# Kernel tuning notes

Hardware: AMD Instinct MI355X
Metric: run time of the kernel (lower is better)

## Reference

```python
import jax, jax.numpy as jnp
import numpy as np
import math

B, L, DIM, DEPTH, HEADS, DH, T, BUCKETS, MAXDIST = 256, 77, 768, 12, 12, 64, 1000, 32, 128
INNER = HEADS * DH            # 768
FF_IN = 4 * DIM               # 3072 (SwiGLU inner)
EPS = 1e-5


def rmsnorm(x, gamma):
    inv = jax.lax.rsqrt(jnp.sum(x * x, axis=-1, keepdims=True) + EPS)
    return x * inv * gamma * (DIM ** 0.5)


def rel_pos_bias(i, j, table):
    # table: [BUCKETS, HEADS] -> bias [HEADS, i, j]
    q_pos = jnp.arange(i)
    k_pos = jnp.arange(j)
    rel = k_pos[None, :] - q_pos[:, None]
    n = jnp.maximum(-rel, 0)
    max_exact = BUCKETS // 2
    is_small = n < max_exact
    nf = jnp.maximum(n, 1).astype(jnp.float32)
    val_large = max_exact + (jnp.log(nf / max_exact) / math.log(MAXDIST / max_exact) * (BUCKETS - max_exact)).astype(jnp.int32)
    val_large = jnp.minimum(val_large, BUCKETS - 1)
    bucket = jnp.where(is_small, n, val_large)
    return jnp.transpose(table[bucket], (2, 0, 1))  # h i j


def attention(x, mask, bias, gamma, Wq, Wkv, Wout, null_kv):
    b, n, _ = x.shape
    xn = rmsnorm(x, gamma)
    q = (xn @ Wq).reshape(b, n, HEADS, DH).transpose(0, 2, 1, 3)     # b h n d
    kv = xn @ Wkv                                                     # b n 2d (single head)
    k, v = kv[..., :DH], kv[..., DH:]
    nk = jnp.broadcast_to(null_kv[0], (b, 1, DH))
    nv = jnp.broadcast_to(null_kv[1], (b, 1, DH))
    k = jnp.concatenate([nk, k], axis=1)                              # b (n+1) d
    v = jnp.concatenate([nv, v], axis=1)
    sim = jnp.einsum('bhid,bjd->bhij', q * (DH ** -0.5), k) + bias[None]
    neg = -jnp.finfo(sim.dtype).max
    m = jnp.pad(mask, ((0, 0), (1, 0)), constant_values=True)         # null kv always visible
    sim = jnp.where(m[:, None, None, :], sim, neg)
    i, j = n, n + 1
    causal = jnp.arange(j)[None, :] > (jnp.arange(i)[:, None] + (j - i))
    sim = jnp.where(causal[None, None], neg, sim)
    attn = jax.nn.softmax(sim - jax.lax.stop_gradient(sim.max(axis=-1, keepdims=True)), axis=-1)
    out = jnp.einsum('bhij,bjd->bhid', attn, v)
    out = out.transpose(0, 2, 1, 3).reshape(b, n, INNER)
    return out @ Wout


def feedforward(x, gamma, W1, W2):
    h = rmsnorm(x, gamma) @ W1                                        # b n 2*FF_IN
    a, gate = h[..., :FF_IN], h[..., FF_IN:]
    return (a * jax.nn.silu(gate)) @ W2


def setup_inputs() -> dict:
    key = jax.random.key(0)
    ks = jax.random.split(key, 16)
    s = 0.02
    return {
        'image_embed': jax.random.normal(ks[0], (B, DIM), jnp.float32),
        'text_encodings': jax.random.normal(ks[1], (B, L, DIM), jnp.float32),
        'text_embed': jax.random.normal(ks[2], (B, DIM), jnp.float32),
        'time_emb_table': jax.random.normal(ks[3], (T, DIM), jnp.float32) * s,
        'learned_query': jax.random.normal(ks[4], (DIM,), jnp.float32),
        'rel_bias_table': jax.random.normal(ks[5], (BUCKETS, HEADS), jnp.float32) * s,
        'attn_gamma': jnp.ones((DEPTH, DIM), jnp.float32),
        'Wq': jax.random.normal(ks[6], (DEPTH, DIM, INNER), jnp.float32) * s,
        'Wkv': jax.random.normal(ks[7], (DEPTH, DIM, 2 * DH), jnp.float32) * s,
        'Wout': jax.random.normal(ks[8], (DEPTH, INNER, DIM), jnp.float32) * s,
        'null_kv': jax.random.normal(ks[9], (DEPTH, 2, DH), jnp.float32),
        'ff_gamma': jnp.ones((DEPTH, DIM), jnp.float32),
        'Wff1': jax.random.normal(ks[10], (DEPTH, DIM, 2 * FF_IN), jnp.float32) * s,
        'Wff2': jax.random.normal(ks[11], (DEPTH, FF_IN, DIM), jnp.float32) * s,
        'diffusion_timesteps': jax.random.randint(ks[12], (B,), 0, T),
        'mask': jnp.ones((B, L), dtype=bool),
    }


def reference(image_embed, text_encodings, text_embed, time_emb_table, learned_query,
              rel_bias_table, attn_gamma, Wq, Wkv, Wout, null_kv, ff_gamma, Wff1, Wff2,
              diffusion_timesteps, mask):
    b = image_embed.shape[0]
    # mask bookkeeping (matches torch forward); cond_drop_prob fixed at 1.0 -> keep all
    not_all = jnp.any(mask, axis=-1)
    m = jnp.concatenate([mask, not_all[:, None]], axis=1)
    m = jnp.pad(m, ((0, 0), (0, 2)), constant_values=True)            # [b, L+3]
    time_embed = time_emb_table[diffusion_timesteps][:, None, :]
    queries = jnp.broadcast_to(learned_query, (b, 1, DIM))
    tokens = jnp.concatenate([text_encodings, text_embed[:, None, :], time_embed, queries], axis=1)
    n = tokens.shape[1]
    bias = rel_pos_bias(n, n + 1, rel_bias_table)
    x = tokens
    for l in range(DEPTH):
        x = attention(x, m, bias, attn_gamma[l], Wq[l], Wkv[l], Wout[l], null_kv[l]) + x
        x = feedforward(x, ff_gamma[l], Wff1[l], Wff2[l]) + x
    return x[:, -1, :]
```

## Files before the change

### kernel.cpp

```cpp
#include <hip/hip_runtime.h>
#include <hip/hip_bf16.h>
#include <float.h>
#include <math.h>

#define NB 256
#define LTXT 77
#define DIM 768
#define DEPTH 12
#define HEADS 12
#define DH 64
#define NTOK 80
#define NKEY 81
#define NROWS (NB*NTOK)
#define FFH 3072
#define FF2C 6144
#define INNER 768
#define SROW 100

typedef __hip_bfloat16 bf16;
typedef __attribute__((ext_vector_type(8))) short short8;
typedef __attribute__((ext_vector_type(4))) float f32x4;

__device__ __forceinline__ unsigned short f2bf(float f) {
    __hip_bfloat16 h = __float2bfloat16(f);
    return __builtin_bit_cast(unsigned short, h);
}

__global__ void build_tokens(const float* __restrict__ text_enc,
                             const float* __restrict__ text_emb,
                             const float* __restrict__ time_tab,
                             const float* __restrict__ lquery,
                             const int* __restrict__ tsteps,
                             float* __restrict__ x) {
    int idx = blockIdx.x * 256 + threadIdx.x;
    if (idx >= NROWS * DIM) return;
    int d = idx % DIM;
    int row = idx / DIM;
    int b = row / NTOK, p = row % NTOK;
    float v;
    if (p < LTXT)            v = text_enc[((size_t)b * LTXT + p) * DIM + d];
    else if (p == LTXT)      v = text_emb[(size_t)b * DIM + d];
    else if (p == LTXT + 1)  v = time_tab[(size_t)tsteps[b] * DIM + d];
    else                     v = lquery[d];
    x[idx] = v;
}

__global__ void build_biasR(const float* __restrict__ table, float* __restrict__ biasR) {
    int idx = blockIdx.x * 256 + threadIdx.x;
    if (idx >= HEADS * NTOK * 96) return;
    int kap = idx % 96;
    int i = (idx / 96) % NTOK;
    int h = idx / (96 * NTOK);
    float v;
    if ((kap < 80 && kap > i) || kap > 80) {
        v = -1e30f;
    } else {
        int j = (kap < 80) ? kap + 1 : 0;
        int rel = j - i;
        int n = rel < 0 ? -rel : 0;
        int bucket;
        if (n < 16) {
            bucket = n;
        } else {
            float val = logf((float)n / 16.0f) / logf(8.0f) * 16.0f;
            int vl = 16 + (int)val;
            bucket = vl < 31 ? vl : 31;
        }
        v = table[bucket * HEADS + h];
    }
    biasR[idx] = v;
}

__global__ __launch_bounds__(256) void convT(const float* __restrict__ W,
                                             bf16* __restrict__ WT,
                                             int K, int N) {
    __shared__ float t[32][33];
    int n0 = blockIdx.x * 32, k0 = blockIdx.y * 32;
    int tx = threadIdx.x & 31, ty = threadIdx.x >> 5;
    #pragma unroll
    for (int i = 0; i < 4; i++)
        t[ty + 8 * i][tx] = W[(size_t)(k0 + ty + 8 * i) * N + n0 + tx];
    __syncthreads();
    #pragma unroll
    for (int i = 0; i < 4; i++)
        WT[(size_t)(n0 + ty + 8 * i) * K + k0 + tx] = __float2bfloat16(t[tx][ty + 8 * i]);
}

__global__ __launch_bounds__(256) void rmsnorm_w(const float* __restrict__ x,
                                                 const float* __restrict__ gamma,
                                                 bf16* __restrict__ out) {
    int wave = blockIdx.x * 4 + (threadIdx.x >> 6);
    int lane = threadIdx.x & 63;
    float4 g0 = *(const float4*)&gamma[lane * 4];
    float4 g1 = *(const float4*)&gamma[lane * 4 + 256];
    float4 g2 = *(const float4*)&gamma[lane * 4 + 512];
    #pragma unroll 2
    for (int rr = 0; rr < 8; ++rr) {
        int row = wave * 8 + rr;
        const float* xr = x + (size_t)row * DIM + lane * 4;
        float4 v0 = *(const float4*)xr;
        float4 v1 = *(const float4*)(xr + 256);
        float4 v2 = *(const float4*)(xr + 512);
        float ss = v0.x*v0.x + v0.y*v0.y + v0.z*v0.z + v0.w*v0.w
                 + v1.x*v1.x + v1.y*v1.y + v1.z*v1.z + v1.w*v1.w
                 + v2.x*v2.x + v2.y*v2.y + v2.z*v2.z + v2.w*v2.w;
        #pragma unroll
        for (int o = 32; o > 0; o >>= 1) ss += __shfl_xor(ss, o);
        float inv = 27.712812921102035f / sqrtf(ss + 1e-5f);
        bf16* orow = out + (size_t)row * DIM + lane * 4;
        ushort4 w0 = { f2bf(v0.x*inv*g0.x), f2bf(v0.y*inv*g0.y), f2bf(v0.z*inv*g0.z), f2bf(v0.w*inv*g0.w) };
        ushort4 w1 = { f2bf(v1.x*inv*g1.x), f2bf(v1.y*inv*g1.y), f2bf(v1.z*inv*g1.z), f2bf(v1.w*inv*g1.w) };
        ushort4 w2 = { f2bf(v2.x*inv*g2.x), f2bf(v2.y*inv*g2.y), f2bf(v2.z*inv*g2.z), f2bf(v2.w*inv*g2.w) };
        *(ushort4*)(orow)       = w0;
        *(ushort4*)(orow + 256) = w1;
        *(ushort4*)(orow + 512) = w2;
    }
}


#define STAGE_LOAD(dst, base, b0, ld)                                          \
    _Pragma("unroll")                                                          \
    for (int r_ = 0; r_ < 4; ++r_) {                                           \
        int idx_ = r_ * 256 + t;                                               \
        int row_ = idx_ >> 3, c_ = idx_ & 7;                                   \
        dst[r_] = *(const short8*)&base[(size_t)(b0 + row_) * ld + k0 + c_ * 8];\
    }

#define STAGE_WRITE(lds, src)                                                  \
    _Pragma("unroll")                                                          \
    for (int r_ = 0; r_ < 4; ++r_) {                                           \
        int idx_ = r_ * 256 + t;                                               \
        int row_ = idx_ >> 3, c_ = idx_ & 7;                                   \
        *(short8*)((char*)lds + row_ * 128 + ((c_ ^ (row_ & 7)) << 4)) = src[r_];\
    }

#define FRAG_READ(dst, lds, base_row, kk)                                      \
    _Pragma("unroll")                                                          \
    for (int q_ = 0; q_ < 4; ++q_) {                                           \
        int row_ = (base_row) + q_ * 16 + fr;                                  \
        dst[q_] = *(const short8*)((const char*)lds + row_ * 128 +             \
                     ((((kk << 2) + kb) ^ (row_ & 7)) << 4));                  \
    }

template<int EPI>
__global__ __launch_bounds__(256) void gemm_bt(const bf16* __restrict__ A,
                                               const bf16* __restrict__ BT,
                                               float* __restrict__ C,
                                               int N, int K) {
    __shared__ __align__(16) short As[128 * 64];
    __shared__ __align__(16) short Bs[128 * 64];
    const int t = threadIdx.x;
    const int lane = t & 63;
    const int wid = t >> 6;
    const int wr = wid >> 1, wc = wid & 1;
    const int fr = lane & 15;
    const int kb = lane >> 4;
    const int row0 = blockIdx.y * 128, col0 = blockIdx.x * 128;

    f32x4 acc[4][4] = {};
    short8 ra[4], rb[4];
    const int NKT = K >> 6;

    int k0 = 0;
    STAGE_LOAD(ra, A, row0, K)
    STAGE_LOAD(rb, BT, col0, K)
    STAGE_WRITE(As, ra)
    STAGE_WRITE(Bs, rb)
    __syncthreads();

    for (int kt = 1; kt < NKT; ++kt) {
        k0 = kt << 6;
        STAGE_LOAD(ra, A, row0, K)
        STAGE_LOAD(rb, BT, col0, K)
        #pragma unroll
        for (int kk = 0; kk < 2; ++kk) {
            short8 af[4], bv[4];
            FRAG_READ(af, As, wr * 64, kk)
            FRAG_READ(bv, Bs, wc * 64, kk)
            #pragma unroll
            for (int i = 0; i < 4; ++i)
                #pragma unroll
                for (int j = 0; j < 4; ++j)
                    acc[i][j] = __builtin_amdgcn_mfma_f32_16x16x32_bf16(af[i], bv[j], acc[i][j], 0, 0, 0);
        }
        __syncthreads();
        STAGE_WRITE(As, ra)
        STAGE_WRITE(Bs, rb)
        __syncthreads();
    }
    #pragma unroll
    for (int kk = 0; kk < 2; ++kk) {
        short8 af[4], bv[4];
        FRAG_READ(af, As, wr * 64, kk)
        FRAG_READ(bv, Bs, wc * 64, kk)
        #pragma unroll
        for (int i = 0; i < 4; ++i)
            #pragma unroll
            for (int j = 0; j < 4; ++j)
                acc[i][j] = __builtin_amdgcn_mfma_f32_16x16x32_bf16(af[i], bv[j], acc[i][j], 0, 0, 0);
    }

    #pragma unroll
    for (int i = 0; i < 4; ++i) {
        #pragma unroll
        for (int j = 0; j < 4; ++j) {
            int row = row0 + wr * 64 + i * 16 + kb * 4;
            int col = col0 + wc * 64 + j * 16 + fr;
            #pragma unroll
            for (int r = 0; r < 4; ++r) {
                size_t o = (size_t)(row + r) * N + col;
                if (EPI == 1)      C[o] += acc[i][j][r];
                else               ((bf16*)C)[o] = __float2bfloat16(acc[i][j][r]);
            }
        }
    }
}

__global__ __launch_bounds__(256) void gemm_kv(const bf16* __restrict__ A,
                                               const bf16* __restrict__ BT,
                                               bf16* __restrict__ kb,
                                               bf16* __restrict__ vT) {
    __shared__ __align__(16) short As[128 * 64];
    __shared__ __align__(16) short Bs[128 * 64];
    const int t = threadIdx.x;
    const int lane = t & 63;
    const int wid = t >> 6;
    const int wr = wid >> 1, wc = wid & 1;
    const int fr = lane & 15;
    const int kb_ = lane >> 4;
    const int row0 = blockIdx.y * 128, col0 = 0;
    const int K = DIM, N = 128;
    #define kb_frag kb_

    f32x4 acc[4][4] = {};
    short8 ra[4], rb[4];

    int k0 = 0;
    STAGE_LOAD(ra, A, row0, K)
    STAGE_LOAD(rb, BT, col0, K)
    STAGE_WRITE(As, ra)
    STAGE_WRITE(Bs, rb)
    __syncthreads();

    for (int kt = 1; kt < (DIM >> 6); ++kt) {
        k0 = kt << 6;
        STAGE_LOAD(ra, A, row0, K)
        STAGE_LOAD(rb, BT, col0, K)
        #pragma unroll
        for (int kk = 0; kk < 2; ++kk) {
            short8 af[4], bv[4];
            {
                _Pragma("unroll")
                for (int q_ = 0; q_ < 4; ++q_) {
                    int row_ = wr * 64 + q_ * 16 + fr;
                    af[q_] = *(const short8*)((const char*)As + row_ * 128 + ((((kk << 2) + kb_) ^ (row_ & 7)) << 4));
                }
                _Pragma("unroll")
                for (int q_ = 0; q_ < 4; ++q_) {
                    int row_ = wc * 64 + q_ * 16 + fr;
                    bv[q_] = *(const short8*)((const char*)Bs + row_ * 128 + ((((kk << 2) + kb_) ^ (row_ & 7)) << 4));
                }
            }
            #pragma unroll
            for (int i = 0; i < 4; ++i)
                #pragma unroll
                for (int j = 0; j < 4; ++j)
                    acc[i][j] = __builtin_amdgcn_mfma_f32_16x16x32_bf16(af[i], bv[j], acc[i][j], 0, 0, 0);
        }
        __syncthreads();
        STAGE_WRITE(As, ra)
        STAGE_WRITE(Bs, rb)
        __syncthreads();
    }
    #pragma unroll
    for (int kk = 0; kk < 2; ++kk) {
        short8 af[4], bv[4];
        _Pragma("unroll")
        for (int q_ = 0; q_ < 4; ++q_) {
            int row_ = wr * 64 + q_ * 16 + fr;
            af[q_] = *(const short8*)((const char*)As + row_ * 128 + ((((kk << 2) + kb_) ^ (row_ & 7)) << 4));
        }
        _Pragma("unroll")
        for (int q_ = 0; q_ < 4; ++q_) {
            int row_ = wc * 64 + q_ * 16 + fr;
            bv[q_] = *(const short8*)((const char*)Bs + row_ * 128 + ((((kk << 2) + kb_) ^ (row_ & 7)) << 4));
        }
        #pragma unroll
        for (int i = 0; i < 4; ++i)
            #pragma unroll
            for (int j = 0; j < 4; ++j)
                acc[i][j] = __builtin_amdgcn_mfma_f32_16x16x32_bf16(af[i], bv[j], acc[i][j], 0, 0, 0);
    }

    #pragma unroll
    for (int i = 0; i < 4; ++i) {
        #pragma unroll
        for (int j = 0; j < 4; ++j) {
            int row = row0 + wr * 64 + i * 16 + kb_ * 4;
            int col = wc * 64 + j * 16 + fr;
            #pragma unroll
            for (int r = 0; r < 4; ++r) {
                int rg = row + r;
                float v = acc[i][j][r];
                if (wc == 0) {
                    kb[(size_t)rg * 64 + col] = __float2bfloat16(v);
                } else {
                    int bb = rg / NTOK, ii = rg - bb * NTOK;
                    vT[((size_t)bb * 64 + (col - 64)) * NTOK + ii] = __float2bfloat16(v);
                }
            }
        }
    }
    #undef kb_frag
}

__global__ __launch_bounds__(256) void attn_mfma(const bf16* __restrict__ qb,
                                                 const bf16* __restrict__ kbuf,
                                                 const bf16* __restrict__ vT,
                                                 const float* __restrict__ nullkv,
                                                 const float* __restrict__ biasR,
                                                 bf16* __restrict__ attnb) {
    const int b = blockIdx.x / HEADS;
    const int h = blockIdx.x % HEADS;
    __shared__ __align__(16) short Ks[96 * 64];
    __shared__ __align__(16) short Vt[64 * 128];
    __shared__ __align__(16) float Sls[80 * SROW];
    char* Sb = (char*)Sls;
    const int t = threadIdx.x;
    const int lane = t & 63;
    const int wid = t >> 6;
    const int g = lane >> 4;
    const int fr = lane & 15;

    for (int c = t; c < 768; c += 256) {
        int row = c >> 3, ch = c & 7;
        short8 v;
        if (row < NTOK) {
            v = *(const short8*)&kbuf[((size_t)(b * NTOK + row)) * 64 + ch * 8];
        } else if (row == NTOK) {
            #pragma unroll
            for (int e = 0; e < 8; ++e) v[e] = (short)f2bf(nullkv[ch * 8 + e]);
        } else {
            v = short8{0,0,0,0,0,0,0,0};
        }
        *(short8*)((char*)Ks + row * 128 + ((ch ^ (row & 7)) << 4)) = v;
    }
    for (int c = t; c < 1024; c += 256) {
        int d = c >> 4, ch = c & 15;
        if (ch >= 12) continue;
        short8 v;
        if (ch < 10) {
            v = *(const short8*)&vT[((size_t)b * 64 + d) * NTOK + ch * 8];
        } else if (ch == 10) {
            v = short8{0,0,0,0,0,0,0,0};
            v[0] = (short)f2bf(nullkv[64 + d]);
        } else {
            v = short8{0,0,0,0,0,0,0,0};
        }
        *(short8*)((char*)Vt + d * 256 + ((ch ^ (d & 7)) << 4)) = v;
    }
    __syncthreads();

    const bf16* qbase = qb + ((size_t)(b * NTOK)) * INNER + h * DH;
    for (int s = 0; s < 8; ++s) {
        int tt = wid + 4 * s;
        if (tt >= 30) break;
        int m = tt / 6, n = tt - 6 * m;
        f32x4 acc = {};
        #pragma unroll
        for (int kk = 0; kk < 2; ++kk) {
            short8 a = *(const short8*)&qbase[(size_t)(m * 16 + fr) * INNER + kk * 32 + g * 8];
            int krow = n * 16 + fr;
            short8 kf = *(const short8*)((const char*)Ks + krow * 128 + ((((kk << 2) + g) ^ (krow & 7)) << 4));
            acc = __builtin_amdgcn_mfma_f32_16x16x32_bf16(a, kf, acc, 0, 0, 0);
        }
        int i0 = m * 16 + g * 4;
        int kap = n * 16 + fr;
        const float* bR = biasR + ((size_t)h * NTOK + i0) * 96 + kap;
        #pragma unroll
        for (int r = 0; r < 4; ++r)
            Sls[(i0 + r) * SROW + kap] = acc[r] * 0.125f + bR[r * 96];
    }
    __syncthreads();

    for (int rr = 0; rr < 20; ++rr) {
        int row = wid + 4 * rr;
        const float* Srow = Sls + row * SROW;
        float s0 = Srow[lane];
        float s1v = Srow[64 + (lane & 31)];
        float mx = fmaxf(s0, s1v);
        #pragma unroll
        for (int o = 32; o > 0; o >>= 1) mx = fmaxf(mx, __shfl_xor(mx, o));
        float e0 = __expf(s0 - mx);
        float e1 = (lane < 32) ? __expf(s1v - mx) : 0.0f;
        float sum = e0 + e1;
        #pragma unroll
        for (int o = 32; o > 0; o >>= 1) sum += __shfl_xor(sum, o);
        float inv = 1.0f / sum;
        *(unsigned short*)(Sb + row * (SROW * 4) + lane * 2) = f2bf(e0 * inv);
        if (lane < 32)
            *(unsigned short*)(Sb + row * (SROW * 4) + 128 + lane * 2) = f2bf(e1 * inv);
    }
    __syncthreads();

    for (int s = 0; s < 5; ++s) {
        int tt = wid + 4 * s;
        int m = tt >> 2, n = tt & 3;
        f32x4 acc = {};
        #pragma unroll
        for (int kc = 0; kc < 3; ++kc) {
            short8 p = *(const short8*)(Sb + (m * 16 + fr) * (SROW * 4) + kc * 64 + g * 16);
            int drow = n * 16 + fr;
            short8 vv = *(const short8*)((const char*)Vt + drow * 256 + ((((kc << 2) + g) ^ (drow & 7)) << 4));
            acc = __builtin_amdgcn_mfma_f32_16x16x32_bf16(p, vv, acc, 0, 0, 0);
        }
        int i0 = m * 16 + g * 4;
        int d = n * 16 + fr;
        #pragma unroll
        for (int r = 0; r < 4; ++r)
            attnb[((size_t)(b * NTOK) + i0 + r) * INNER + h * DH + d] = __float2bfloat16(acc[r]);
    }
}

__global__ __launch_bounds__(256) void gemm_ff1(const bf16* __restrict__ A,
                                                const bf16* __restrict__ W1T,
                                                bf16* __restrict__ act) {
    __shared__ __align__(16) short As[128 * 64];
    __shared__ __align__(16) short Bs1[128 * 64];
    __shared__ __align__(16) short Bs2[128 * 64];
    const int t = threadIdx.x;
    const int lane = t & 63;
    const int wid = t >> 6;
    const int wr = wid >> 1, wc = wid & 1;
    const int fr = lane & 15;
    const int kb = lane >> 4;
    const int row0 = blockIdx.y * 128, col0 = blockIdx.x * 128;
    const int K = DIM;
    const bf16* B1 = W1T;
    const bf16* B2 = W1T + (size_t)FFH * DIM;

    f32x4 acc1[4][4] = {}, acc2[4][4] = {};
    short8 ra[4], rb1[4], rb2[4];

    int k0 = 0;
    STAGE_LOAD(ra, A, row0, K)
    STAGE_LOAD(rb1, B1, col0, K)
    STAGE_LOAD(rb2, B2, col0, K)
    STAGE_WRITE(As, ra)
    STAGE_WRITE(Bs1, rb1)
    STAGE_WRITE(Bs2, rb2)
    __syncthreads();

    for (int kt = 1; kt < (DIM >> 6); ++kt) {
        k0 = kt << 6;
        STAGE_LOAD(ra, A, row0, K)
        STAGE_LOAD(rb1, B1, col0, K)
        STAGE_LOAD(rb2, B2, col0, K)
        #pragma unroll
        for (int kk = 0; kk < 2; ++kk) {
            short8 af[4], b1v[4], b2v[4];
            FRAG_READ(af, As, wr * 64, kk)
            FRAG_READ(b1v, Bs1, wc * 64, kk)
            FRAG_READ(b2v, Bs2, wc * 64, kk)
            #pragma unroll
            for (int i = 0; i < 4; ++i)
                #pragma unroll
                for (int j = 0; j < 4; ++j) {
                    acc1[i][j] = __builtin_amdgcn_mfma_f32_16x16x32_bf16(af[i], b1v[j], acc1[i][j], 0, 0, 0);
                    acc2[i][j] = __builtin_amdgcn_mfma_f32_16x16x32_bf16(af[i], b2v[j], acc2[i][j], 0, 0, 0);
                }
        }
        __syncthreads();
        STAGE_WRITE(As, ra)
        STAGE_WRITE(Bs1, rb1)
        STAGE_WRITE(Bs2, rb2)
        __syncthreads();
    }
    #pragma unroll
    for (int kk = 0; kk < 2; ++kk) {
        short8 af[4], b1v[4], b2v[4];
        FRAG_READ(af, As, wr * 64, kk)
        FRAG_READ(b1v, Bs1, wc * 64, kk)
        FRAG_READ(b2v, Bs2, wc * 64, kk)
        #pragma unroll
        for (int i = 0; i < 4; ++i)
            #pragma unroll
            for (int j = 0; j < 4; ++j) {
                acc1[i][j] = __builtin_amdgcn_mfma_f32_16x16x32_bf16(af[i], b1v[j], acc1[i][j], 0, 0, 0);
                acc2[i][j] = __builtin_amdgcn_mfma_f32_16x16x32_bf16(af[i], b2v[j], acc2[i][j], 0, 0, 0);
            }
    }

    #pragma unroll
    for (int i = 0; i < 4; ++i) {
        #pragma unroll
        for (int j = 0; j < 4; ++j) {
            int row = row0 + wr * 64 + i * 16 + kb * 4;
            int col = col0 + wc * 64 + j * 16 + fr;
            #pragma unroll
            for (int r = 0; r < 4; ++r) {
                float a = acc1[i][j][r];
                float gt = acc2[i][j][r];
                float s = a * gt / (1.0f + __expf(-gt));
                act[(size_t)(row + r) * FFH + col] = __float2bfloat16(s);
            }
        }
    }
}

__global__ void extract(const float* __restrict__ x, float* __restrict__ out) {
    int idx = blockIdx.x * 256 + threadIdx.x;
    if (idx >= NB * DIM) return;
    int b = idx / DIM, d = idx % DIM;
    out[idx] = x[((size_t)(b * NTOK + NTOK - 1)) * DIM + d];
}

extern "C" void kernel_launch(void* const* d_in, const int* in_sizes, int n_in,
                              void* d_out, int out_size, void* d_ws, size_t ws_size,
                              hipStream_t stream) {
    (void)in_sizes; (void)n_in; (void)out_size; (void)ws_size;
    const float* text_enc = (const float*)d_in[1];
    const float* text_emb = (const float*)d_in[2];
    const float* time_tab = (const float*)d_in[3];
    const float* lquery   = (const float*)d_in[4];
    const float* rel_tab  = (const float*)d_in[5];
    const float* attn_g   = (const float*)d_in[6];
    const float* Wq       = (const float*)d_in[7];
    const float* Wkv      = (const float*)d_in[8];
    const float* Wout     = (const float*)d_in[9];
    const float* null_kv  = (const float*)d_in[10];
    const float* ff_g     = (const float*)d_in[11];
    const float* Wff1     = (const float*)d_in[12];
    const float* Wff2     = (const float*)d_in[13];
    const int*   tsteps   = (const int*)d_in[14];

    char* ws = (char*)d_ws;
    float* x     = (float*)(ws);
    bf16*  xn    = (bf16*)(ws + 62914560);
    bf16*  attnb = xn;
    char*  U     = ws + 94371840;
    bf16*  qb    = (bf16*)U;
    bf16*  kbuf  = (bf16*)(U + 31457280);
    bf16*  vT    = (bf16*)(U + 34078720);
    bf16*  act   = (bf16*)U;
    float* biasR = (float*)(ws + 220200960);
    bf16*  WqT   = (bf16*)(ws + 220569600);
    bf16*  WkvT  = (bf16*)(ws + 221749248);
    bf16*  WoutT = (bf16*)(ws + 221945856);
    bf16*  Wff1T = (bf16*)(ws + 223125504);
    bf16*  Wff2T = (bf16*)(ws + 232562688);

    build_tokens<<<(NROWS * DIM + 255) / 256, 256, 0, stream>>>(text_enc, text_emb, time_tab, lquery, tsteps, x);
    build_biasR<<<(HEADS * NTOK * 96 + 255) / 256, 256, 0, stream>>>(rel_tab, biasR);

    for (int l = 0; l < DEPTH; l++) {
        convT<<<dim3(INNER / 32, DIM / 32), 256, 0, stream>>>(Wq   + (size_t)l * DIM * INNER,  WqT,   DIM,   INNER);
        convT<<<dim3((2 * DH) / 32, DIM / 32), 256, 0, stream>>>(Wkv + (size_t)l * DIM * 2 * DH, WkvT, DIM, 2 * DH);
        convT<<<dim3(DIM / 32, INNER / 32), 256, 0, stream>>>(Wout + (size_t)l * INNER * DIM,  WoutT, INNER, DIM);
        convT<<<dim3(FF2C / 32, DIM / 32), 256, 0, stream>>>(Wff1 + (size_t)l * DIM * FF2C,    Wff1T, DIM,   FF2C);
        convT<<<dim3(DIM / 32, FFH / 32), 256, 0, stream>>>(Wff2  + (size_t)l * FFH * DIM,     Wff2T, FFH,   DIM);

        rmsnorm_w<<<NROWS / (8 * 4), 256, 0, stream>>>(x, attn_g + (size_t)l * DIM, xn);
        gemm_bt<2><<<dim3(INNER / 128, NROWS / 128), 256, 0, stream>>>(xn, WqT, (float*)qb, INNER, DIM);
        gemm_kv<<<dim3(1, NROWS / 128), 256, 0, stream>>>(xn, WkvT, kbuf, vT);
        attn_mfma<<<NB * HEADS, 256, 0, stream>>>(qb, kbuf, vT, null_kv + (size_t)l * 2 * DH, biasR, attnb);
        gemm_bt<1><<<dim3(DIM / 128, NROWS / 128), 256, 0, stream>>>(attnb, WoutT, x, DIM, INNER);

        rmsnorm_w<<<NROWS / (8 * 4), 256, 0, stream>>>(x, ff_g + (size_t)l * DIM, xn);
        gemm_ff1<<<dim3(FFH / 128, NROWS / 128), 256, 0, stream>>>(xn, Wff1T, act);
        gemm_bt<1><<<dim3(DIM / 128, NROWS / 128), 256, 0, stream>>>(act, Wff2T, x, DIM, FFH);
    }

    extract<<<(NB * DIM + 255) / 256, 256, 0, stream>>>(x, (float*)d_out);
}
```

Baseline: 9.137 ms.

## Load GEMM tiles directly into LDS with global_load_lds, dropping register prefetch

```diff
diff --git a/kernel.cpp b/kernel.cpp
--- a/kernel.cpp
+++ b/kernel.cpp
@@ -118,28 +118,25 @@
 }
 
 
-#define STAGE_LOAD(dst, base, b0, ld)                                          \
+#define GSTAGE(lds, base, b0, ld)                                              \
     _Pragma("unroll")                                                          \
     for (int r_ = 0; r_ < 4; ++r_) {                                           \
         int idx_ = r_ * 256 + t;                                               \
         int row_ = idx_ >> 3, c_ = idx_ & 7;                                   \
-        dst[r_] = *(const short8*)&base[(size_t)(b0 + row_) * ld + k0 + c_ * 8];\
-    }
-
-#define STAGE_WRITE(lds, src)                                                  \
-    _Pragma("unroll")                                                          \
-    for (int r_ = 0; r_ < 4; ++r_) {                                           \
-        int idx_ = r_ * 256 + t;                                               \
-        int row_ = idx_ >> 3, c_ = idx_ & 7;                                   \
-        *(short8*)((char*)lds + row_ * 128 + ((c_ ^ (row_ & 7)) << 4)) = src[r_];\
+        int cs_ = c_ ^ (row_ & 7);                                             \
+        __builtin_amdgcn_global_load_lds(                                      \
+            (const __attribute__((address_space(1))) unsigned int*)            \
+                &base[(size_t)(b0 + row_) * ld + k0 + cs_ * 8],                \
+            (__attribute__((address_space(3))) unsigned int*)&lds[idx_ * 8],   \
+            16, 0, 0);                                                         \
     }
 
 #define FRAG_READ(dst, lds, base_row, kk)                                      \
     _Pragma("unroll")                                                          \
     for (int q_ = 0; q_ < 4; ++q_) {                                           \
         int row_ = (base_row) + q_ * 16 + fr;                                  \
-        dst[q_] = *(const short8*)((const char*)lds + row_ * 128 +             \
-                     ((((kk << 2) + kb) ^ (row_ & 7)) << 4));                  \
+        int ch_ = ((((kk) << 2) + kb) ^ (row_ & 7));                           \
+        dst[q_] = *(const short8*)&lds[row_ * 64 + ch_ * 8];                   \
     }
 
 template<int EPI>
@@ -158,20 +155,13 @@
     const int row0 = blockIdx.y * 128, col0 = blockIdx.x * 128;
 
     f32x4 acc[4][4] = {};
-    short8 ra[4], rb[4];
     const int NKT = K >> 6;
 
-    int k0 = 0;
-    STAGE_LOAD(ra, A, row0, K)
-    STAGE_LOAD(rb, BT, col0, K)
-    STAGE_WRITE(As, ra)
-    STAGE_WRITE(Bs, rb)
-    __syncthreads();
-
-    for (int kt = 1; kt < NKT; ++kt) {
-        k0 = kt << 6;
-        STAGE_LOAD(ra, A, row0, K)
-        STAGE_LOAD(rb, BT, col0, K)
+    for (int kt = 0; kt < NKT; ++kt) {
+        int k0 = kt << 6;
+        GSTAGE(As, A, row0, K)
+        GSTAGE(Bs, BT, col0, K)
+        __syncthreads();
         #pragma unroll
         for (int kk = 0; kk < 2; ++kk) {
             short8 af[4], bv[4];
@@ -184,20 +174,6 @@
                     acc[i][j] = __builtin_amdgcn_mfma_f32_16x16x32_bf16(af[i], bv[j], acc[i][j], 0, 0, 0);
         }
         __syncthreads();
-        STAGE_WRITE(As, ra)
-        STAGE_WRITE(Bs, rb)
-        __syncthreads();
-    }
-    #pragma unroll
-    for (int kk = 0; kk < 2; ++kk) {
-        short8 af[4], bv[4];
-        FRAG_READ(af, As, wr * 64, kk)
-        FRAG_READ(bv, Bs, wc * 64, kk)
-        #pragma unroll
-        for (int i = 0; i < 4; ++i)
-            #pragma unroll
-            for (int j = 0; j < 4; ++j)
-                acc[i][j] = __builtin_amdgcn_mfma_f32_16x16x32_bf16(af[i], bv[j], acc[i][j], 0, 0, 0);
     }
 
     #pragma unroll
@@ -218,7 +194,7 @@
 
 __global__ __launch_bounds__(256) void gemm_kv(const bf16* __restrict__ A,
                                                const bf16* __restrict__ BT,
-                                               bf16* __restrict__ kb,
+                                               bf16* __restrict__ kout,
                                                bf16* __restrict__ vT) {
     __shared__ __align__(16) short As[128 * 64];
     __shared__ __align__(16) short Bs[128 * 64];
@@ -227,40 +203,22 @@
     const int wid = t >> 6;
     const int wr = wid >> 1, wc = wid & 1;
     const int fr = lane & 15;
-    const int kb_ = lane >> 4;
-    const int row0 = blockIdx.y * 128, col0 = 0;
-    const int K = DIM, N = 128;
-    #define kb_frag kb_
+    const int kb = lane >> 4;
+    const int row0 = blockIdx.y * 128;
+    const int K = DIM;
 
     f32x4 acc[4][4] = {};
-    short8 ra[4], rb[4];
-
-    int k0 = 0;
-    STAGE_LOAD(ra, A, row0, K)
-    STAGE_LOAD(rb, BT, col0, K)
-    STAGE_WRITE(As, ra)
-    STAGE_WRITE(Bs, rb)
-    __syncthreads();
-
-    for (int kt = 1; kt < (DIM >> 6); ++kt) {
-        k0 = kt << 6;
-        STAGE_LOAD(ra, A, row0, K)
-        STAGE_LOAD(rb, BT, col0, K)
+
+    for (int kt = 0; kt < (DIM >> 6); ++kt) {
+        int k0 = kt << 6;
+        GSTAGE(As, A, row0, K)
+        GSTAGE(Bs, BT, 0, K)
+        __syncthreads();
         #pragma unroll
         for (int kk = 0; kk < 2; ++kk) {
             short8 af[4], bv[4];
-            {
-                _Pragma("unroll")
-                for (int q_ = 0; q_ < 4; ++q_) {
-                    int row_ = wr * 64 + q_ * 16 + fr;
-                    af[q_] = *(const short8*)((const char*)As + row_ * 128 + ((((kk << 2) + kb_) ^ (row_ & 7)) << 4));
-                }
-                _Pragma("unroll")
-                for (int q_ = 0; q_ < 4; ++q_) {
-                    int row_ = wc * 64 + q_ * 16 + fr;
-                    bv[q_] = *(const short8*)((const char*)Bs + row_ * 128 + ((((kk << 2) + kb_) ^ (row_ & 7)) << 4));
-                }
-            }
+            FRAG_READ(af, As, wr * 64, kk)
+            FRAG_READ(bv, Bs, wc * 64, kk)
             #pragma unroll
             for (int i = 0; i < 4; ++i)
                 #pragma unroll
@@ -268,42 +226,20 @@
                     acc[i][j] = __builtin_amdgcn_mfma_f32_16x16x32_bf16(af[i], bv[j], acc[i][j], 0, 0, 0);
         }
         __syncthreads();
-        STAGE_WRITE(As, ra)
-        STAGE_WRITE(Bs, rb)
-        __syncthreads();
-    }
-    #pragma unroll
-    for (int kk = 0; kk < 2; ++kk) {
-        short8 af[4], bv[4];
-        _Pragma("unroll")
-        for (int q_ = 0; q_ < 4; ++q_) {
-            int row_ = wr * 64 + q_ * 16 + fr;
-            af[q_] = *(const short8*)((const char*)As + row_ * 128 + ((((kk << 2) + kb_) ^ (row_ & 7)) << 4));
-        }
-        _Pragma("unroll")
-        for (int q_ = 0; q_ < 4; ++q_) {
-            int row_ = wc * 64 + q_ * 16 + fr;
-            bv[q_] = *(const short8*)((const char*)Bs + row_ * 128 + ((((kk << 2) + kb_) ^ (row_ & 7)) << 4));
-        }
-        #pragma unroll
-        for (int i = 0; i < 4; ++i)
-            #pragma unroll
-            for (int j = 0; j < 4; ++j)
-                acc[i][j] = __builtin_amdgcn_mfma_f32_16x16x32_bf16(af[i], bv[j], acc[i][j], 0, 0, 0);
     }
 
     #pragma unroll
     for (int i = 0; i < 4; ++i) {
         #pragma unroll
         for (int j = 0; j < 4; ++j) {
-            int row = row0 + wr * 64 + i * 16 + kb_ * 4;
+            int row = row0 + wr * 64 + i * 16 + kb * 4;
             int col = wc * 64 + j * 16 + fr;
             #pragma unroll
             for (int r = 0; r < 4; ++r) {
                 int rg = row + r;
                 float v = acc[i][j][r];
                 if (wc == 0) {
-                    kb[(size_t)rg * 64 + col] = __float2bfloat16(v);
+                    kout[(size_t)rg * 64 + col] = __float2bfloat16(v);
                 } else {
                     int bb = rg / NTOK, ii = rg - bb * NTOK;
                     vT[((size_t)bb * 64 + (col - 64)) * NTOK + ii] = __float2bfloat16(v);
@@ -311,7 +247,6 @@
             }
         }
     }
-    #undef kb_frag
 }
 
 __global__ __launch_bounds__(256) void attn_mfma(const bf16* __restrict__ qb,
@@ -440,22 +375,13 @@
     const bf16* B2 = W1T + (size_t)FFH * DIM;
 
     f32x4 acc1[4][4] = {}, acc2[4][4] = {};
-    short8 ra[4], rb1[4], rb2[4];
-
-    int k0 = 0;
-    STAGE_LOAD(ra, A, row0, K)
-    STAGE_LOAD(rb1, B1, col0, K)
-    STAGE_LOAD(rb2, B2, col0, K)
-    STAGE_WRITE(As, ra)
-    STAGE_WRITE(Bs1, rb1)
-    STAGE_WRITE(Bs2, rb2)
-    __syncthreads();
-
-    for (int kt = 1; kt < (DIM >> 6); ++kt) {
-        k0 = kt << 6;
-        STAGE_LOAD(ra, A, row0, K)
-        STAGE_LOAD(rb1, B1, col0, K)
-        STAGE_LOAD(rb2, B2, col0, K)
+
+    for (int kt = 0; kt < (DIM >> 6); ++kt) {
+        int k0 = kt << 6;
+        GSTAGE(As, A, row0, K)
+        GSTAGE(Bs1, B1, col0, K)
+        GSTAGE(Bs2, B2, col0, K)
+        __syncthreads();
         #pragma unroll
         for (int kk = 0; kk < 2; ++kk) {
             short8 af[4], b1v[4], b2v[4];
@@ -471,24 +397,6 @@
                 }
         }
         __syncthreads();
-        STAGE_WRITE(As, ra)
-        STAGE_WRITE(Bs1, rb1)
-        STAGE_WRITE(Bs2, rb2)
-        __syncthreads();
-    }
-    #pragma unroll
-    for (int kk = 0; kk < 2; ++kk) {
-        short8 af[4], b1v[4], b2v[4];
-        FRAG_READ(af, As, wr * 64, kk)
-        FRAG_READ(b1v, Bs1, wc * 64, kk)
-        FRAG_READ(b2v, Bs2, wc * 64, kk)
-        #pragma unroll
-        for (int i = 0; i < 4; ++i)
-            #pragma unroll
-            for (int j = 0; j < 4; ++j) {
-                acc1[i][j] = __builtin_amdgcn_mfma_f32_16x16x32_bf16(af[i], b1v[j], acc1[i][j], 0, 0, 0);
-                acc2[i][j] = __builtin_amdgcn_mfma_f32_16x16x32_bf16(af[i], b2v[j], acc2[i][j], 0, 0, 0);
-            }
     }
 
     #pragma unroll
```

Result: slower. 9.585 ms (+4.9%).
